# Kernel tuning notes

Measured on AMD Instinct MI355X. Metric: run time of the kernel, lower is better.

The kernel has to match this reference:

```python
import jax, jax.numpy as jnp
import numpy as np

ANCHORS = np.array([[10,13],[16,30],[33,23],[30,61],[62,45],[59,119],[116,90],[156,198],[373,326]], dtype=np.float32)
ANCHOR_MASK = [[6,7,8],[3,4,5],[0,1,2]]
CLASS_NUM = 80
IGNORE_THRESH = 0.5


def _bce_mean(z, x):
    # Keras BinaryCrossentropy(from_logits=True) called as a loss object:
    # elementwise sigmoid-CE, mean over last axis, then SUM_OVER_BATCH_SIZE
    # reduction == mean over ALL elements -> scalar.
    ce = jnp.maximum(x, 0.0) - x * z + jnp.log1p(jnp.exp(-jnp.abs(x)))
    return jnp.mean(ce)


def _layer_loss(out, lab, anchors):
    B, gh, gw, _ = out.shape
    A = anchors.shape[0]
    feats = out.reshape(B, gh, gw, A, CLASS_NUM + 5)
    anchors = jnp.asarray(anchors, dtype=jnp.float32)  # [A,2] (w,h)
    inp_wh = jnp.array([gw * 32, gh * 32], dtype=jnp.float32)  # reverse(input_shape)
    grid_wh = jnp.array([gw, gh], dtype=jnp.float32)           # reverse(grid_shape)

    gy, gx = jnp.meshgrid(jnp.arange(gh), jnp.arange(gw), indexing='ij')
    grid = jnp.stack([gx, gy], axis=-1).astype(jnp.float32)[:, :, None, :]  # [gh,gw,1,2]

    pred_xy = (jax.nn.sigmoid(feats[..., 0:2]) + grid) / grid_wh
    pred_wh = jnp.exp(feats[..., 2:4]) * anchors / inp_wh
    pred_box = jnp.concatenate([pred_xy, pred_wh], axis=-1)  # [B,gh,gw,A,4]

    obj = lab[..., 4:5]          # [B,gh,gw,A,1]
    objb = obj != 0.0
    N = gh * gw * A

    def _per_image(args):
        pb, tb, valid = args  # pb: [N,4] predicted, tb: [N,4] label boxes, valid: [N] bool
        b1_xy, b1_wh = pb[:, None, 0:2], pb[:, None, 2:4]
        b2_xy, b2_wh = tb[None, :, 0:2], tb[None, :, 2:4]
        b1_mins, b1_maxes = b1_xy - b1_wh / 2.0, b1_xy + b1_wh / 2.0
        b2_mins, b2_maxes = b2_xy - b2_wh / 2.0, b2_xy + b2_wh / 2.0
        inter_mins = jnp.maximum(b1_mins, b2_mins)
        inter_maxes = jnp.maximum(b1_maxes, b2_maxes)  # faithful to source (uses maximum, not minimum)
        inter_wh = jnp.maximum(inter_maxes - inter_mins, 0.0)
        inter = inter_wh[..., 0] * inter_wh[..., 1]
        a1 = b1_wh[..., 0] * b1_wh[..., 1]
        a2 = b2_wh[..., 0] * b2_wh[..., 1]
        iou = inter / (a1 + a2 - inter)  # [N,N]
        # only true boxes count; empty set -> best=-1 (matches tf reduce_max of empty = -inf)
        iou = jnp.where(valid[None, :], iou, -1.0)
        best_iou = jnp.max(iou, axis=-1)
        return (best_iou < IGNORE_THRESH).astype(jnp.float32)

    ignore = jax.lax.map(_per_image, (pred_box.reshape(B, N, 4),
                                      lab[..., 0:4].reshape(B, N, 4),
                                      objb.reshape(B, N)))
    ignore = jax.lax.stop_gradient(ignore).reshape(B, gh, gw, A, 1)

    raw_true_xy = lab[..., 0:2] * grid_wh - grid
    raw_true_wh = jnp.log(lab[..., 2:4] * inp_wh / anchors)
    raw_true_wh = jnp.where(objb, raw_true_wh, 0.0)
    box_loss_scale = 2.0 - lab[..., 2:3] * lab[..., 3:4]

    bf = jnp.float32(B)
    xy_loss = jnp.sum(obj * box_loss_scale * _bce_mean(raw_true_xy, feats[..., 0:2])) / bf
    wh_loss = jnp.sum(obj * box_loss_scale * 0.5 * jnp.square(raw_true_wh - feats[..., 2:4])) / bf
    conf_bce = _bce_mean(obj, feats[..., 4:5])
    conf_loss = jnp.sum(obj * conf_bce + (1.0 - obj) * conf_bce * ignore) / bf
    class_loss = jnp.sum(obj * _bce_mean(lab[..., 5:], feats[..., 5:])) / bf
    return xy_loss + wh_loss + conf_loss + class_loss


def _make_labels(key, B, g):
    k1, k2, k3, k4 = jax.random.split(key, 4)
    xy = jax.random.uniform(k1, (B, g, g, 3, 2), dtype=jnp.float32)
    wh = jax.random.uniform(k2, (B, g, g, 3, 2), dtype=jnp.float32, minval=0.05, maxval=1.0)
    objness = (jax.random.uniform(k3, (B, g, g, 3, 1)) < 0.02).astype(jnp.float32)
    cls = (jax.random.uniform(k4, (B, g, g, 3, CLASS_NUM)) < 0.05).astype(jnp.float32)
    return jnp.concatenate([xy, wh, objness, cls], axis=-1)


def setup_inputs() -> dict:
    key = jax.random.key(0)
    ks = jax.random.split(key, 6)
    B = 8
    grids = [13, 26, 52]
    out = {}
    for i, g in enumerate(grids):
        out[f'o{i}'] = jax.random.normal(ks[i], (B, g, g, 3 * (CLASS_NUM + 5)), dtype=jnp.float32)
        out[f'l{i}'] = _make_labels(ks[3 + i], B, g)
    return out


def reference(o0, o1, o2, l0, l1, l2):
    outputs = (o0, o1, o2)
    labels = (l0, l1, l2)
    loss = jnp.float32(0.0)
    for l in range(3):
        loss = loss + _layer_loss(outputs[l], labels[l], ANCHORS[ANCHOR_MASK[l]])
    return loss
```

## Files before the change

### kernel.cpp

```cpp
#include <hip/hip_runtime.h>
#include <math.h>

#define BDIM 256

__device__ __constant__ float c_aw[3][3] = {{116.f,156.f,373.f},{30.f,62.f,59.f},{10.f,16.f,33.f}};
__device__ __constant__ float c_ah[3][3] = {{90.f,198.f,326.f},{61.f,45.f,119.f},{13.f,30.f,23.f}};


__device__ __forceinline__ float bce(float z, float x) {
    return fmaxf(x, 0.f) - x * z + log1pf(expf(-fabsf(x)));
}

__device__ __forceinline__ void decode_blk(int blk, int& layer, int& blk0) {
    if (blk < 16)      { layer = 0; blk0 = 0; }
    else if (blk < 80) { layer = 1; blk0 = 16; }
    else               { layer = 2; blk0 = 80; }
}

__global__ __launch_bounds__(BDIM) void pass_a(
    const float* __restrict__ o0, const float* __restrict__ l0,
    const float* __restrict__ o1, const float* __restrict__ l1,
    const float* __restrict__ o2, const float* __restrict__ l2,
    double* __restrict__ acc, int* __restrict__ cnt, float4* __restrict__ tbox)
{
    int layer, blk0;
    decode_blk(blockIdx.x, layer, blk0);
    const int g     = (layer == 0) ? 13 : (layer == 1) ? 26 : 52;
    const int C     = 8 * g * g * 3;
    const int Nl    = g * g * 3;
    const int tbase = (layer == 0) ? 0 : (layer == 1) ? 4056 : 20280;
    const float* O  = (layer == 0) ? o0 : (layer == 1) ? o1 : o2;
    const float* L  = (layer == 0) ? l0 : (layer == 1) ? l1 : l2;

    int cell = (blockIdx.x - blk0) * BDIM + (int)threadIdx.x;
    float s_xy = 0.f, s_wh = 0.f, s_conf = 0.f, s_cls = 0.f, s_obj = 0.f, s_s1 = 0.f;
    if (cell < C) {
        int a  = cell % 3;
        int xi = (cell / 3) % g;
        int yi = (cell / (3 * g)) % g;
        int b  = cell / (3 * g * g);
        const float* op = O + (size_t)cell * 85;
        const float* lp = L + (size_t)cell * 85;
        float tx = op[0], ty = op[1], tw = op[2], th = op[3], tc = op[4];
        float lx = lp[0], ly = lp[1], lw = lp[2], lh = lp[3], lobj = lp[4];
        float gf = (float)g;
        float rtx = lx * gf - (float)xi;
        float rty = ly * gf - (float)yi;
        s_xy = bce(rtx, tx) + bce(rty, ty);
        bool objb = (lobj != 0.f);
        float aw = c_aw[layer][a], ah = c_ah[layer][a];
        float inp = gf * 32.f;
        float rtw = objb ? logf(lw * inp / aw) : 0.f;
        float rth = objb ? logf(lh * inp / ah) : 0.f;
        float bls = 2.f - lw * lh;
        float dw = rtw - tw, dh = rth - th;
        s_wh   = lobj * bls * 0.5f * (dw * dw + dh * dh);
        s_conf = bce(lobj, tc);
        s_obj  = lobj;
        s_s1   = lobj * bls;
        float cl = 0.f;
        #pragma unroll 8
        for (int k = 0; k < 80; k++) cl += bce(lp[5 + k], op[5 + k]);
        s_cls = cl;
        if (objb) {
            int idx = atomicAdd(&cnt[layer * 8 + b], 1);
            tbox[tbase + b * Nl + idx] = make_float4(lx, ly, lw, lh);
        }
    }
    __shared__ float sb[6][4];
    float v[6] = {s_xy, s_wh, s_conf, s_cls, s_obj, s_s1};
    #pragma unroll
    for (int q = 0; q < 6; q++) {
        float x = v[q];
        #pragma unroll
        for (int off = 32; off > 0; off >>= 1) x += __shfl_down(x, off, 64);
        if ((threadIdx.x & 63) == 0) sb[q][threadIdx.x >> 6] = x;
    }
    __syncthreads();
    if (threadIdx.x < 6) {
        int q = threadIdx.x;
        double s = (double)sb[q][0] + (double)sb[q][1] + (double)sb[q][2] + (double)sb[q][3];
        atomicAdd(&acc[layer * 7 + q], s);
    }
}

__global__ __launch_bounds__(BDIM) void pass_b(
    const float* __restrict__ o0, const float* __restrict__ l0,
    const float* __restrict__ o1, const float* __restrict__ l1,
    const float* __restrict__ o2, const float* __restrict__ l2,
    double* __restrict__ acc, const int* __restrict__ cnt, const float4* __restrict__ tbox)
{
    int layer, blk0;
    decode_blk(blockIdx.x, layer, blk0);
    const int g     = (layer == 0) ? 13 : (layer == 1) ? 26 : 52;
    const int C     = 8 * g * g * 3;
    const int Nl    = g * g * 3;
    const int tbase = (layer == 0) ? 0 : (layer == 1) ? 4056 : 20280;
    const float* O  = (layer == 0) ? o0 : (layer == 1) ? o1 : o2;
    const float* L  = (layer == 0) ? l0 : (layer == 1) ? l1 : l2;

    int cell = (blockIdx.x - blk0) * BDIM + (int)threadIdx.x;
    float v = 0.f;
    if (cell < C) {
        int a  = cell % 3;
        int xi = (cell / 3) % g;
        int yi = (cell / (3 * g)) % g;
        int b  = cell / (3 * g * g);
        const float* op = O + (size_t)cell * 85;
        float tx = op[0], ty = op[1], tw = op[2], th = op[3];
        float lobj = L[(size_t)cell * 85 + 4];
        float gf = (float)g, inp = gf * 32.f;
        float aw = c_aw[layer][a], ah = c_ah[layer][a];
        float px = (1.f / (1.f + expf(-tx)) + (float)xi) / gf;
        float py = (1.f / (1.f + expf(-ty)) + (float)yi) / gf;
        float pw = expf(tw) * aw / inp;
        float ph = expf(th) * ah / inp;
        float pminx = px - pw * 0.5f, pmaxx = px + pw * 0.5f;
        float pminy = py - ph * 0.5f, pmaxy = py + ph * 0.5f;
        float a1 = pw * ph;
        int n = cnt[layer * 8 + b];
        const float4* tp = tbox + tbase + b * Nl;
        float best = -1.f;
        for (int j = 0; j < n; j++) {
            float4 t = tp[j];
            float hw = t.z * 0.5f, hh = t.w * 0.5f;
            float imnx = fmaxf(pminx, t.x - hw);
            float imxx = fmaxf(pmaxx, t.x + hw);
            float imny = fmaxf(pminy, t.y - hh);
            float imxy = fmaxf(pmaxy, t.y + hh);
            float iw = fmaxf(imxx - imnx, 0.f);
            float ih = fmaxf(imxy - imny, 0.f);
            float inter = iw * ih;
            float iou = inter / (a1 + t.z * t.w - inter);
            best = fmaxf(best, iou);
        }
        v = (best < 0.5f) ? (1.f - lobj) : 0.f;
    }
    __shared__ float sb[4];
    float x = v;
    #pragma unroll
    for (int off = 32; off > 0; off >>= 1) x += __shfl_down(x, off, 64);
    if ((threadIdx.x & 63) == 0) sb[threadIdx.x >> 6] = x;
    __syncthreads();
    if (threadIdx.x == 0) {
        double s = (double)sb[0] + (double)sb[1] + (double)sb[2] + (double)sb[3];
        atomicAdd(&acc[layer * 7 + 6], s);
    }
}

__global__ void finalize_k(const double* __restrict__ acc, float* __restrict__ out)
{
    if (threadIdx.x == 0 && blockIdx.x == 0) {
        double loss = 0.0;
        const int gs[3] = {13, 26, 52};
        for (int l = 0; l < 3; l++) {
            double C   = 8.0 * gs[l] * gs[l] * 3.0;
            double bxy = acc[l * 7 + 0] / (C * 2.0);
            double wh  = acc[l * 7 + 1];
            double cf  = acc[l * 7 + 2] / C;
            double cm  = acc[l * 7 + 3] / (C * 80.0);
            double ob  = acc[l * 7 + 4];
            double s1  = acc[l * 7 + 5];
            double ni  = acc[l * 7 + 6];
            loss += (bxy * s1 + wh + cf * (ob + ni) + cm * ob) / 8.0;
        }
        out[0] = (float)loss;
    }
}

extern "C" void kernel_launch(void* const* d_in, const int* in_sizes, int n_in,
                              void* d_out, int out_size, void* d_ws, size_t ws_size,
                              hipStream_t stream)
{
    const float* o0 = (const float*)d_in[0];
    const float* l0 = (const float*)d_in[1];
    const float* o1 = (const float*)d_in[2];
    const float* l1 = (const float*)d_in[3];
    const float* o2 = (const float*)d_in[4];
    const float* l2 = (const float*)d_in[5];

    double* acc  = (double*)d_ws;
    int*    cnt  = (int*)((char*)d_ws + 192);
    float4* tbox = (float4*)((char*)d_ws + 512);

    hipMemsetAsync(d_ws, 0, 512, stream);
    pass_a<<<334, BDIM, 0, stream>>>(o0, l0, o1, l1, o2, l2, acc, cnt, tbox);
    pass_b<<<334, BDIM, 0, stream>>>(o0, l0, o1, l1, o2, l2, acc, cnt, tbox);
    finalize_k<<<1, 64, 0, stream>>>(acc, (float*)d_out);
}
```

Measured before the change: 172.6 us.

## Coalesce pass_a with float4 element streaming and precompute boxes for IoU pass

pass_a now walks the output and label tensors element-wise as float4 loads with a grid-stride loop over many more blocks, instead of having one thread read a whole 85-float cell, so the global loads are coalesced. It writes decoded predicted boxes and the no-object weight to workspace. pass_b becomes per-image: it stages true boxes in shared memory, exits early once an IoU of 0.5 or more is found, and reads the precomputed boxes instead of reloading raw tensors. The cost is per-element div/mod by 85, divergent branches, scattered writes of pbox components, and extra workspace traffic.

New measurement: 215.9 us. +25.1%, slower.

```diff
diff --git a/kernel.cpp b/kernel.cpp
--- a/kernel.cpp
+++ b/kernel.cpp
@@ -9,64 +9,86 @@
 
 __device__ __forceinline__ float bce(float z, float x) {
     return fmaxf(x, 0.f) - x * z + log1pf(expf(-fabsf(x)));
-}
-
-__device__ __forceinline__ void decode_blk(int blk, int& layer, int& blk0) {
-    if (blk < 16)      { layer = 0; blk0 = 0; }
-    else if (blk < 80) { layer = 1; blk0 = 16; }
-    else               { layer = 2; blk0 = 80; }
 }
 
 __global__ __launch_bounds__(BDIM) void pass_a(
     const float* __restrict__ o0, const float* __restrict__ l0,
     const float* __restrict__ o1, const float* __restrict__ l1,
     const float* __restrict__ o2, const float* __restrict__ l2,
-    double* __restrict__ acc, int* __restrict__ cnt, float4* __restrict__ tbox)
-{
-    int layer, blk0;
-    decode_blk(blockIdx.x, layer, blk0);
+    double* __restrict__ acc, int* __restrict__ cnt, float4* __restrict__ tbox,
+    float4* __restrict__ pbox, float* __restrict__ noobj)
+{
+    int layer, blk0, nblk;
+    if (blockIdx.x < 64)       { layer = 0; blk0 = 0;   nblk = 64;   }
+    else if (blockIdx.x < 384) { layer = 1; blk0 = 64;  nblk = 320;  }
+    else                       { layer = 2; blk0 = 384; nblk = 1408; }
     const int g     = (layer == 0) ? 13 : (layer == 1) ? 26 : 52;
-    const int C     = 8 * g * g * 3;
-    const int Nl    = g * g * 3;
-    const int tbase = (layer == 0) ? 0 : (layer == 1) ? 4056 : 20280;
+    const int Nlimg = g * g * 3;
+    const int n4    = 8 * Nlimg * 85 / 4;
+    const int cbase = (layer == 0) ? 0 : (layer == 1) ? 4056 : 20280;
     const float* O  = (layer == 0) ? o0 : (layer == 1) ? o1 : o2;
     const float* L  = (layer == 0) ? l0 : (layer == 1) ? l1 : l2;
-
-    int cell = (blockIdx.x - blk0) * BDIM + (int)threadIdx.x;
+    const float4* O4 = (const float4*)O;
+    const float4* L4 = (const float4*)L;
+    const float gf = (float)g;
+    const float inp = gf * 32.f;
+
     float s_xy = 0.f, s_wh = 0.f, s_conf = 0.f, s_cls = 0.f, s_obj = 0.f, s_s1 = 0.f;
-    if (cell < C) {
-        int a  = cell % 3;
-        int xi = (cell / 3) % g;
-        int yi = (cell / (3 * g)) % g;
-        int b  = cell / (3 * g * g);
-        const float* op = O + (size_t)cell * 85;
-        const float* lp = L + (size_t)cell * 85;
-        float tx = op[0], ty = op[1], tw = op[2], th = op[3], tc = op[4];
-        float lx = lp[0], ly = lp[1], lw = lp[2], lh = lp[3], lobj = lp[4];
-        float gf = (float)g;
-        float rtx = lx * gf - (float)xi;
-        float rty = ly * gf - (float)yi;
-        s_xy = bce(rtx, tx) + bce(rty, ty);
-        bool objb = (lobj != 0.f);
-        float aw = c_aw[layer][a], ah = c_ah[layer][a];
-        float inp = gf * 32.f;
-        float rtw = objb ? logf(lw * inp / aw) : 0.f;
-        float rth = objb ? logf(lh * inp / ah) : 0.f;
-        float bls = 2.f - lw * lh;
-        float dw = rtw - tw, dh = rth - th;
-        s_wh   = lobj * bls * 0.5f * (dw * dw + dh * dh);
-        s_conf = bce(lobj, tc);
-        s_obj  = lobj;
-        s_s1   = lobj * bls;
-        float cl = 0.f;
-        #pragma unroll 8
-        for (int k = 0; k < 80; k++) cl += bce(lp[5 + k], op[5 + k]);
-        s_cls = cl;
-        if (objb) {
-            int idx = atomicAdd(&cnt[layer * 8 + b], 1);
-            tbox[tbase + b * Nl + idx] = make_float4(lx, ly, lw, lh);
+
+    for (int i4 = (int)(blockIdx.x - blk0) * BDIM + (int)threadIdx.x; i4 < n4;
+         i4 += nblk * BDIM) {
+        float4 ov = O4[i4];
+        float4 lv = L4[i4];
+        int e0 = i4 * 4;
+        float vo[4] = {ov.x, ov.y, ov.z, ov.w};
+        float vl[4] = {lv.x, lv.y, lv.z, lv.w};
+        #pragma unroll
+        for (int j = 0; j < 4; j++) {
+            int e    = e0 + j;
+            int cell = e / 85;
+            int c    = e - cell * 85;
+            float x = vo[j], z = vl[j];
+            if (c >= 5) {
+                s_cls += bce(z, x);
+            } else if (c == 4) {
+                s_conf += bce(z, x);
+                s_obj  += z;
+                noobj[cbase + cell] = 1.f - z;
+                if (z != 0.f) {
+                    float lx = L[(size_t)cell * 85 + 0];
+                    float ly = L[(size_t)cell * 85 + 1];
+                    float lw = L[(size_t)cell * 85 + 2];
+                    float lh = L[(size_t)cell * 85 + 3];
+                    s_s1 += z * (2.f - lw * lh);
+                    int b = cell / Nlimg;
+                    int idx = atomicAdd(&cnt[layer * 8 + b], 1);
+                    tbox[cbase + b * Nlimg + idx] = make_float4(lx, ly, lw, lh);
+                }
+            } else if (c < 2) {
+                int xi = (cell / 3) % g;
+                int yi = (cell / (3 * g)) % g;
+                float coord = (c == 0) ? (float)xi : (float)yi;
+                float rt = z * gf - coord;
+                s_xy += bce(rt, x);
+                ((float*)pbox)[(size_t)(cbase + cell) * 4 + c] =
+                    (1.f / (1.f + expf(-x)) + coord) / gf;
+            } else {
+                int a = cell % 3;
+                float an = (c == 2) ? c_aw[layer][a] : c_ah[layer][a];
+                float lobj = L[(size_t)cell * 85 + 4];
+                if (lobj != 0.f) {
+                    float other = L[(size_t)cell * 85 + (c == 2 ? 3 : 2)];
+                    float lw = (c == 2) ? z : other;
+                    float lh = (c == 2) ? other : z;
+                    float rt = logf(z * inp / an);
+                    float d = rt - x;
+                    s_wh += lobj * (2.f - lw * lh) * 0.5f * d * d;
+                }
+                ((float*)pbox)[(size_t)(cbase + cell) * 4 + c] = expf(x) * an / inp;
+            }
         }
     }
+
     __shared__ float sb[6][4];
     float v[6] = {s_xy, s_wh, s_conf, s_cls, s_obj, s_s1};
     #pragma unroll
@@ -84,58 +106,62 @@
     }
 }
 
+#define TCAP 512
 __global__ __launch_bounds__(BDIM) void pass_b(
-    const float* __restrict__ o0, const float* __restrict__ l0,
-    const float* __restrict__ o1, const float* __restrict__ l1,
-    const float* __restrict__ o2, const float* __restrict__ l2,
-    double* __restrict__ acc, const int* __restrict__ cnt, const float4* __restrict__ tbox)
-{
-    int layer, blk0;
-    decode_blk(blockIdx.x, layer, blk0);
+    double* __restrict__ acc, const int* __restrict__ cnt,
+    const float4* __restrict__ tbox, const float4* __restrict__ pbox,
+    const float* __restrict__ noobj)
+{
+    int layer, img, chunk;
+    if (blockIdx.x < 16)      { layer = 0; img = blockIdx.x >> 1; chunk = blockIdx.x & 1; }
+    else if (blockIdx.x < 80) { int t = blockIdx.x - 16; layer = 1; img = t >> 3; chunk = t & 7; }
+    else                      { int t = blockIdx.x - 80; layer = 2; img = t >> 5; chunk = t & 31; }
     const int g     = (layer == 0) ? 13 : (layer == 1) ? 26 : 52;
-    const int C     = 8 * g * g * 3;
-    const int Nl    = g * g * 3;
-    const int tbase = (layer == 0) ? 0 : (layer == 1) ? 4056 : 20280;
-    const float* O  = (layer == 0) ? o0 : (layer == 1) ? o1 : o2;
-    const float* L  = (layer == 0) ? l0 : (layer == 1) ? l1 : l2;
-
-    int cell = (blockIdx.x - blk0) * BDIM + (int)threadIdx.x;
-    float v = 0.f;
-    if (cell < C) {
-        int a  = cell % 3;
-        int xi = (cell / 3) % g;
-        int yi = (cell / (3 * g)) % g;
-        int b  = cell / (3 * g * g);
-        const float* op = O + (size_t)cell * 85;
-        float tx = op[0], ty = op[1], tw = op[2], th = op[3];
-        float lobj = L[(size_t)cell * 85 + 4];
-        float gf = (float)g, inp = gf * 32.f;
-        float aw = c_aw[layer][a], ah = c_ah[layer][a];
-        float px = (1.f / (1.f + expf(-tx)) + (float)xi) / gf;
-        float py = (1.f / (1.f + expf(-ty)) + (float)yi) / gf;
-        float pw = expf(tw) * aw / inp;
-        float ph = expf(th) * ah / inp;
-        float pminx = px - pw * 0.5f, pmaxx = px + pw * 0.5f;
-        float pminy = py - ph * 0.5f, pmaxy = py + ph * 0.5f;
-        float a1 = pw * ph;
-        int n = cnt[layer * 8 + b];
-        const float4* tp = tbox + tbase + b * Nl;
-        float best = -1.f;
-        for (int j = 0; j < n; j++) {
-            float4 t = tp[j];
-            float hw = t.z * 0.5f, hh = t.w * 0.5f;
-            float imnx = fmaxf(pminx, t.x - hw);
-            float imxx = fmaxf(pmaxx, t.x + hw);
-            float imny = fmaxf(pminy, t.y - hh);
-            float imxy = fmaxf(pmaxy, t.y + hh);
-            float iw = fmaxf(imxx - imnx, 0.f);
-            float ih = fmaxf(imxy - imny, 0.f);
-            float inter = iw * ih;
-            float iou = inter / (a1 + t.z * t.w - inter);
-            best = fmaxf(best, iou);
+    const int Nlimg = g * g * 3;
+    const int cbase = (layer == 0) ? 0 : (layer == 1) ? 4056 : 20280;
+
+    int ci = chunk * BDIM + (int)threadIdx.x;
+    bool live = (ci < Nlimg);
+    int cell = cbase + img * Nlimg + (live ? ci : 0);
+
+    float pminx = 0, pmaxx = 0, pminy = 0, pmaxy = 0, a1 = 0, nb = 0;
+    if (live) {
+        float4 p = pbox[cell];
+        pminx = p.x - p.z * 0.5f; pmaxx = p.x + p.z * 0.5f;
+        pminy = p.y - p.w * 0.5f; pmaxy = p.y + p.w * 0.5f;
+        a1 = p.z * p.w;
+        nb = noobj[cell];
+    }
+    int n = cnt[layer * 8 + img];
+    const float4* tp = tbox + cbase + img * Nlimg;
+
+    __shared__ float4 sT[TCAP];
+    float best = -1.f;
+    bool done = !live;
+    for (int t0 = 0; t0 < n; t0 += TCAP) {
+        int tn = min(TCAP, n - t0);
+        __syncthreads();
+        for (int i = threadIdx.x; i < tn; i += BDIM) sT[i] = tp[t0 + i];
+        __syncthreads();
+        if (!done) {
+            for (int j = 0; j < tn; j++) {
+                float4 t = sT[j];
+                float hw = t.z * 0.5f, hh = t.w * 0.5f;
+                float imnx = fmaxf(pminx, t.x - hw);
+                float imxx = fmaxf(pmaxx, t.x + hw);
+                float imny = fmaxf(pminy, t.y - hh);
+                float imxy = fmaxf(pmaxy, t.y + hh);
+                float iw = fmaxf(imxx - imnx, 0.f);
+                float ih = fmaxf(imxy - imny, 0.f);
+                float inter = iw * ih;
+                float iou = inter / (a1 + t.z * t.w - inter);
+                best = fmaxf(best, iou);
+                if (best >= 0.5f) { done = true; break; }
+            }
         }
-        v = (best < 0.5f) ? (1.f - lobj) : 0.f;
-    }
+    }
+    float v = (live && best < 0.5f) ? nb : 0.f;
+
     __shared__ float sb[4];
     float x = v;
     #pragma unroll
@@ -179,12 +205,14 @@
     const float* o2 = (const float*)d_in[4];
     const float* l2 = (const float*)d_in[5];
 
-    double* acc  = (double*)d_ws;
-    int*    cnt  = (int*)((char*)d_ws + 192);
-    float4* tbox = (float4*)((char*)d_ws + 512);
+    double* acc   = (double*)d_ws;
+    int*    cnt   = (int*)((char*)d_ws + 192);
+    float4* tbox  = (float4*)((char*)d_ws + 512);
+    float4* pbox  = (float4*)((char*)d_ws + 1363328);
+    float*  noobj = (float*)((char*)d_ws + 2726144);
 
     hipMemsetAsync(d_ws, 0, 512, stream);
-    pass_a<<<334, BDIM, 0, stream>>>(o0, l0, o1, l1, o2, l2, acc, cnt, tbox);
-    pass_b<<<334, BDIM, 0, stream>>>(o0, l0, o1, l1, o2, l2, acc, cnt, tbox);
+    pass_a<<<1792, BDIM, 0, stream>>>(o0, l0, o1, l1, o2, l2, acc, cnt, tbox, pbox, noobj);
+    pass_b<<<336, BDIM, 0, stream>>>(acc, cnt, tbox, pbox, noobj);
     finalize_k<<<1, 64, 0, stream>>>(acc, (float*)d_out);
 }
```
